# Optimization experiments

Measured on AMD Instinct MI355X. Metric: run time of the kernel, lower is better.

Reference implementation:

```python
import jax, jax.numpy as jnp
import numpy as np

B, T_X, T_V, F, H, PRED_LEN = 1024, 32, 64, 128, 1024, 64


def setup_inputs() -> dict:
    key = jax.random.key(0)
    ks = jax.random.split(key, 9)
    s = 1.0 / np.sqrt(H)  # PyTorch LSTM/Linear default init range
    return {
        "x": jax.random.normal(ks[0], (B, T_X, F), jnp.float32),
        "y": jax.random.normal(ks[1], (B, PRED_LEN, F), jnp.float32),
        "v": jax.random.normal(ks[2], (B, T_V, F), jnp.float32),
        "W_ih": jax.random.uniform(ks[3], (4 * H, F), jnp.float32, -s, s),
        "W_hh": jax.random.uniform(ks[4], (4 * H, H), jnp.float32, -s, s),
        "b_ih": jax.random.uniform(ks[5], (4 * H,), jnp.float32, -s, s),
        "b_hh": jax.random.uniform(ks[6], (4 * H,), jnp.float32, -s, s),
        "W_reg": jax.random.uniform(ks[7], (F, H), jnp.float32, -s, s),
        "b_reg": jax.random.uniform(ks[8], (F,), jnp.float32, -s, s),
    }


def _lstm_cell(v, h, c, W_ih, W_hh, b):
    # PyTorch gate order: i, f, g, o
    gates = v @ W_ih.T + h @ W_hh.T + b  # [B, 4H]
    i, f, g, o = jnp.split(gates, 4, axis=-1)
    c = jax.nn.sigmoid(f) * c + jax.nn.sigmoid(i) * jnp.tanh(g)
    h = jax.nn.sigmoid(o) * jnp.tanh(c)
    return h, c


def reference(x, y, v, W_ih, W_hh, b_ih, b_hh, W_reg, b_reg):
    # config.scale_x_m / scale_v_m treated as identity (external, undefined).
    b = b_ih + b_hh
    x_last = x[:, -1, :]  # last observed step, [B, F]

    # --- encoder: run LSTM over the full v sequence ---
    v_seq = jnp.transpose(v, (1, 0, 2))  # [T_V, B, F]
    h0 = jnp.zeros((x.shape[0], H), x.dtype)

    def enc_step(carry, vt):
        h, c = carry
        h, c = _lstm_cell(vt, h, c, W_ih, W_hh, b)
        return (h, c), None

    (h, c), _ = jax.lax.scan(enc_step, (h0, h0), v_seq)

    # reg applied to all LSTM outputs then last step taken == reg(h_T)
    v1 = h @ W_reg.T + b_reg  # [B, F]
    x1 = x_last + v1

    def dec_step(carry, _):
        vcur, h, c, xcur = carry
        h, c = _lstm_cell(vcur, h, c, W_ih, W_hh, b)
        vnew = h @ W_reg.T + b_reg
        xnew = xcur + vnew  # x accumulates increments (x += in torch)
        return (vnew, h, c, xnew), xnew

    _, xs = jax.lax.scan(dec_step, (v1, h, c, x1), None, length=PRED_LEN - 1)

    output = jnp.concatenate([x1[None], xs], axis=0)  # [PRED_LEN, B, F]
    y_out = jnp.transpose(y, (1, 0, 2))  # scale_x_m(y.permute(1,0,2)) = identity
    return output, y_out
```

## Files before the change

kernel.cpp:

```cpp
#include <hip/hip_runtime.h>
#include <cstdint>
#include <cstddef>


typedef unsigned short u16;
typedef __bf16 bf16x8 __attribute__((ext_vector_type(8)));
typedef float f32x4 __attribute__((ext_vector_type(4)));

#define DI __device__ __forceinline__

DI u16 f2bf(float x) {
    uint32_t u = __float_as_uint(x);
    u += 0x7fffu + ((u >> 16) & 1u);
    return (u16)(u >> 16);
}
DI float sigm(float x) { return 1.0f / (1.0f + __expf(-x)); }
DI float tanh_(float x) {
    float e = __expf(-2.0f * fabsf(x));
    float r = (1.0f - e) / (1.0f + e);
    return copysignf(r, x);
}

DI void gld16(const void* g, void* l) {
    __builtin_amdgcn_global_load_lds(
        (__attribute__((address_space(1))) void*)(uintptr_t)(g),
        (__attribute__((address_space(3))) void*)(l), 16, 0, 0);
}

DI f32x4 mfma16(bf16x8 a, bf16x8 b, f32x4 c) {
    return __builtin_amdgcn_mfma_f32_16x16x32_bf16(a, b, c, 0, 0, 0);
}

__global__ __launch_bounds__(512, 4)
void lstm_step(const u16* __restrict__ A,
               const u16* __restrict__ W,
               int ldw, int kt0, int ntk,
               const float* __restrict__ bias,
               float* __restrict__ cst,
               u16* __restrict__ Aout,
               u16* __restrict__ hall,
               const float* __restrict__ vsrc)
{
    __shared__ __align__(16) u16 As[2][4096];
    __shared__ __align__(16) u16 Bs[2][8192];
    const int tid  = threadIdx.x;
    const int lane = tid & 63, wave = tid >> 6;
    const int wm = wave >> 1, wn = wave & 1;
    const int l15 = lane & 15, l4 = lane >> 4;

    const int id = blockIdx.x;
    const int xcd = id & 7, slot = id >> 3;
    const int bx = xcd * 4 + (slot >> 4);
    const int by = slot & 15;
    const int u0 = bx << 5, b0 = by << 6;

    f32x4 acc[4] = {};

    const u16* asrc = A + (size_t)(b0 + (wave & 3) * 16 + l15) * 1152
                        + (wave >> 2) * 32 + l4 * 8;
    const u16* bsrc[2];
#pragma unroll
    for (int i = 0; i < 2; ++i) {
        const int fi = i * 8 + wave;
        const int ks = fi >> 3, uh = (fi >> 2) & 1, g = fi & 3;
        bsrc[i] = W + (size_t)(g * 1024 + u0 + uh * 16 + l15) * ldw
                    + ks * 32 + l4 * 8;
    }

#define STAGE(kt, buf)                                                        \
    {                                                                         \
        const size_t ko = (size_t)(kt) * 64;                                  \
        gld16(asrc + ko, (char*)&As[buf][0] + (wave << 10));                  \
        gld16(bsrc[0] + ko, (char*)&Bs[buf][0] + (wave << 10));               \
        gld16(bsrc[1] + ko, (char*)&Bs[buf][0] + ((8 + wave) << 10));         \
    }

    STAGE(kt0, 0);
    __syncthreads();
    int buf = 0;
    for (int kt = kt0; kt < ntk; ++kt) {
        if (kt + 1 < ntk) STAGE(kt + 1, buf ^ 1);
#pragma unroll
        for (int ks = 0; ks < 2; ++ks) {
            const bf16x8 af = *(const bf16x8*)((const char*)&As[buf][0] +
                              (((ks * 4 + wm) * 64 + lane) << 4));
            bf16x8 bfr[4];
#pragma unroll
            for (int g = 0; g < 4; ++g)
                bfr[g] = *(const bf16x8*)((const char*)&Bs[buf][0] +
                         (((ks * 8 + wn * 4 + g) * 64 + lane) << 4));
#pragma unroll
            for (int g = 0; g < 4; ++g)
                acc[g] = mfma16(af, bfr[g], acc[g]);
        }
        __syncthreads();
        buf ^= 1;
    }
#undef STAGE

    const int u = u0 + wn * 16 + l15;
    const float bi = bias[u],        bff = bias[1024 + u],
                bg = bias[2048 + u], bo  = bias[3072 + u];
    const int brow = b0 + wm * 16 + l4 * 4;
#pragma unroll
    for (int j = 0; j < 4; ++j) {
        const int b = brow + j;
        const size_t ci = (size_t)b * 1024 + u;
        const float cold = cst[ci];
        const float xi = acc[0][j] + bi;
        const float xf = acc[1][j] + bff;
        const float xg = acc[2][j] + bg;
        const float xo = acc[3][j] + bo;
        const float cn = sigm(xf) * cold + sigm(xi) * tanh_(xg);
        const float hn = sigm(xo) * tanh_(cn);
        cst[ci] = cn;
        const u16 hb = f2bf(hn);
        Aout[(size_t)b * 1152 + u] = hb;
        if (hall) hall[(size_t)b * 1024 + u] = hb;
    }

    if (vsrc != nullptr && bx == 0) {
        for (int s = tid; s < 2048; s += 512) {
            const int bl = s >> 5, f4 = s & 31;
            const float4 vv = *(const float4*)(vsrc + (size_t)(b0 + bl) * 8192 + f4 * 4);
            ushort4 ov = make_ushort4(f2bf(vv.x), f2bf(vv.y), f2bf(vv.z), f2bf(vv.w));
            *(ushort4*)(Aout + (size_t)(b0 + bl) * 1152 + 1024 + f4 * 4) = ov;
        }
    }
}

__global__ __launch_bounds__(256)
void gemm_nt(const u16* __restrict__ A, int lda,
             const u16* __restrict__ Bw, float* __restrict__ C)
{
    __shared__ __align__(16) u16 As[128 * 64];
    __shared__ __align__(16) u16 Bs[128 * 64];
    const int tid = threadIdx.x, lane = tid & 63, wave = tid >> 6;
    const int wm = wave >> 1, wn = wave & 1;
    const int l15 = lane & 15, l4 = lane >> 4;
    const size_t row0 = (size_t)blockIdx.x * 128;

    f32x4 acc[4][4] = {};
    const u16* asrc[4];
    const u16* bsrc[4];
#pragma unroll
    for (int i = 0; i < 4; ++i) {
        int fi = i * 4 + wave;
        int ks = fi >> 3, rib = fi & 7;
        int r = rib * 16 + l15, k = ks * 32 + l4 * 8;
        asrc[i] = A + (row0 + r) * (size_t)lda + k;
        bsrc[i] = Bw + (size_t)r * 1024 + k;
    }
    for (int kt = 0; kt < 16; ++kt) {
#pragma unroll
        for (int i = 0; i < 4; ++i) {
            gld16(asrc[i] + kt * 64, (char*)As + ((i * 256 + wave * 64) << 4));
            gld16(bsrc[i] + kt * 64, (char*)Bs + ((i * 256 + wave * 64) << 4));
        }
        __syncthreads();
#pragma unroll
        for (int ks = 0; ks < 2; ++ks) {
            bf16x8 af[4], bfr[4];
#pragma unroll
            for (int t = 0; t < 4; ++t) {
                af[t]  = *(const bf16x8*)((const char*)As + (((ks * 8 + wm * 4 + t) * 64 + lane) << 4));
                bfr[t] = *(const bf16x8*)((const char*)Bs + (((ks * 8 + wn * 4 + t) * 64 + lane) << 4));
            }
#pragma unroll
            for (int mi = 0; mi < 4; ++mi)
#pragma unroll
                for (int ni = 0; ni < 4; ++ni)
                    acc[mi][ni] = mfma16(af[mi], bfr[ni], acc[mi][ni]);
        }
        __syncthreads();
    }
#pragma unroll
    for (int mi = 0; mi < 4; ++mi)
#pragma unroll
        for (int ni = 0; ni < 4; ++ni) {
            const int r = wm * 64 + mi * 16 + l4 * 4;
            const int cc = wn * 64 + ni * 16 + l15;
#pragma unroll
            for (int j = 0; j < 4; ++j)
                C[(row0 + r + j) * 128 + cc] = acc[mi][ni][j];
        }
}


__global__ __launch_bounds__(256)
void scan_out(const float* __restrict__ Vall, const float* __restrict__ x,
              const float* __restrict__ breg, float* __restrict__ out)
{
    const int idx = blockIdx.x * 256 + threadIdx.x;
    const int b = idx >> 7, f = idx & 127;
    const float br = breg[f];
    float acc = x[(size_t)b * 4096 + 31 * 128 + f];
    for (int k = 0; k < 64; ++k) {
        acc += Vall[(size_t)k * 131072 + idx] + br;
        out[(size_t)k * 131072 + idx] = acc;
    }
}

__global__ __launch_bounds__(256)
void transpose_y(const float* __restrict__ y, float* __restrict__ out2)
{
    const int idx = blockIdx.x * 256 + threadIdx.x;
    const int f4 = idx & 31;
    const int rest = idx >> 5;
    const int b = rest & 1023, p = rest >> 10;
    const float4 vv = *(const float4*)(y + ((size_t)b * 64 + p) * 128 + f4 * 4);
    *(float4*)(out2 + ((size_t)p * 1024 + b) * 128 + f4 * 4) = vv;
}

__global__ __launch_bounds__(256)
void conv_wcat(const float* __restrict__ Whh, const float* __restrict__ Wih,
               u16* __restrict__ Wcat)
{
    const int idx = blockIdx.x * 256 + threadIdx.x;
    const int j = idx / 288, r = idx % 288;
    const float4 vv = (r < 256)
        ? *(const float4*)(Whh + (size_t)j * 1024 + r * 4)
        : *(const float4*)(Wih + (size_t)j * 128 + (r - 256) * 4);
    ushort4 ov = make_ushort4(f2bf(vv.x), f2bf(vv.y), f2bf(vv.z), f2bf(vv.w));
    *(ushort4*)(Wcat + (size_t)j * 1152 + r * 4) = ov;
}

__global__ __launch_bounds__(256)
void conv_wreg(const float* __restrict__ Wreg, u16* __restrict__ Wregb)
{
    const int idx = blockIdx.x * 256 + threadIdx.x;
    const float4 vv = *(const float4*)(Wreg + (size_t)idx * 4);
    ushort4 ov = make_ushort4(f2bf(vv.x), f2bf(vv.y), f2bf(vv.z), f2bf(vv.w));
    *(ushort4*)(Wregb + (size_t)idx * 4) = ov;
}

__global__ __launch_bounds__(256)
void prep_wdec(const float* __restrict__ Whh, const float* __restrict__ Wih,
               const float* __restrict__ Wreg, const float* __restrict__ bih,
               const float* __restrict__ bhh, const float* __restrict__ breg,
               u16* __restrict__ Wdec, float* __restrict__ bcomb,
               float* __restrict__ bdec)
{
    __shared__ float wih[16][128];
    const int jt = blockIdx.x >> 2, ut = blockIdx.x & 3;
    const int j0 = jt * 16;
    const int u = ut * 256 + threadIdx.x;
    for (int s = threadIdx.x; s < 2048; s += 256)
        wih[s >> 7][s & 127] = Wih[(size_t)(j0 + (s >> 7)) * 128 + (s & 127)];
    __syncthreads();
    float acc[16];
#pragma unroll
    for (int j = 0; j < 16; ++j) acc[j] = Whh[(size_t)(j0 + j) * 1024 + u];
    for (int f = 0; f < 128; ++f) {
        const float wr = Wreg[(size_t)f * 1024 + u];
#pragma unroll
        for (int j = 0; j < 16; ++j) acc[j] += wih[j][f] * wr;
    }
#pragma unroll
    for (int j = 0; j < 16; ++j)
        Wdec[(size_t)(j0 + j) * 1024 + u] = f2bf(acc[j]);
    if (ut == 0 && threadIdx.x < 16) {
        const int j = j0 + threadIdx.x;
        float a = bih[j] + bhh[j];
        bcomb[j] = a;
        for (int f = 0; f < 128; ++f) a += wih[threadIdx.x][f] * breg[f];
        bdec[j] = a;
    }
}

__global__ __launch_bounds__(256)
void init_acat(const float* __restrict__ v, u16* __restrict__ Acat)
{
    const int idx = blockIdx.x * 256 + threadIdx.x;
    const int b = idx >> 5, f4 = idx & 31;
    const float4 vv = *(const float4*)(v + (size_t)b * 8192 + f4 * 4);
    ushort4 ov = make_ushort4(f2bf(vv.x), f2bf(vv.y), f2bf(vv.z), f2bf(vv.w));
    *(ushort4*)(Acat + (size_t)b * 1152 + 1024 + f4 * 4) = ov;
}


extern "C" void kernel_launch(void* const* d_in, const int* in_sizes, int n_in,
                              void* d_out, int out_size, void* d_ws, size_t ws_size,
                              hipStream_t stream)
{
    const float* x    = (const float*)d_in[0];
    const float* y    = (const float*)d_in[1];
    const float* v    = (const float*)d_in[2];
    const float* Wih  = (const float*)d_in[3];
    const float* Whh  = (const float*)d_in[4];
    const float* bih  = (const float*)d_in[5];
    const float* bhh  = (const float*)d_in[6];
    const float* Wreg = (const float*)d_in[7];
    const float* breg = (const float*)d_in[8];
    float* out = (float*)d_out;
    char* ws = (char*)d_ws;

    u16*   Wcat  = (u16*)(ws + 0);
    u16*   Wdec  = (u16*)(ws + 9437184);
    u16*   Wregb = (u16*)(ws + 17825792);
    float* bcomb = (float*)(ws + 18087936);
    float* bdec  = (float*)(ws + 18104320);
    u16*   Ac0   = (u16*)(ws + 18120704);
    u16*   Ac1   = (u16*)(ws + 20480000);
    float* cst   = (float*)(ws + 22839296);
    u16*   Hall  = (u16*)(ws + 27033600);
    float* Vall  = out;
    u16* Ac[2] = {Ac0, Ac1};

    const bool batched = ws_size >= (size_t)27033600 + 134217728;

    hipMemsetAsync(cst, 0, 4194304, stream);
    hipMemsetAsync(Ac0, 0, 2359296, stream);
    prep_wdec<<<1024, 256, 0, stream>>>(Whh, Wih, Wreg, bih, bhh, breg,
                                        Wdec, bcomb, bdec);
    conv_wcat<<<4608, 256, 0, stream>>>(Whh, Wih, Wcat);
    conv_wreg<<<128, 256, 0, stream>>>(Wreg, Wregb);
    init_acat<<<128, 256, 0, stream>>>(v, Ac0);
    transpose_y<<<8192, 256, 0, stream>>>(y, out + 8388608);

    for (int t = 0; t < 64; ++t) {
        lstm_step<<<512, 512, 0, stream>>>(
            Ac[t & 1], Wcat, 1152, (t == 0) ? 16 : 0, 18, bcomb, cst,
            Ac[(t + 1) & 1],
            (batched && t == 63) ? Hall : (u16*)nullptr,
            (t < 63) ? (v + (size_t)(t + 1) * 128) : (const float*)nullptr);
    }
    if (!batched)
        gemm_nt<<<8, 256, 0, stream>>>(Ac[0], 1152, Wregb, Vall);

    for (int k = 1; k < 64; ++k) {
        lstm_step<<<512, 512, 0, stream>>>(
            Ac[(k + 1) & 1], Wdec, 1024, 0, 16, bdec, cst, Ac[k & 1],
            batched ? (Hall + (size_t)k * 1048576) : (u16*)nullptr,
            (const float*)nullptr);
        if (!batched)
            gemm_nt<<<8, 256, 0, stream>>>(Ac[k & 1], 1152, Wregb,
                                           Vall + (size_t)k * 131072);
    }
    if (batched)
        gemm_nt<<<512, 256, 0, stream>>>(Hall, 1024, Wregb, Vall);

    scan_out<<<512, 256, 0, stream>>>(Vall, x, breg, out);
}
```

Baseline: 3.916 ms.

## Enlarge LSTM step tile to 128x128 with triple-buffered LDS pipeline

The per-step LSTM GEMM now uses 256-thread blocks that each compute a 128-batch by 32-unit (times 4 gates) tile, giving each wave a 4x4 grid of MFMA accumulators instead of 1x4. Global-to-LDS loads are triple-buffered, with explicit vmcnt waits and one barrier per k-tile, replacing double buffering with two barriers. The aim is more MFMA work per loaded fragment and better overlap of loads with compute. In exchange the grid is halved to 256 blocks, LDS use rises to 96KB per block, and register pressure grows, so fewer waves are resident on each CU.

```diff
diff --git a/kernel.cpp b/kernel.cpp
--- a/kernel.cpp
+++ b/kernel.cpp
@@ -31,7 +31,7 @@
     return __builtin_amdgcn_mfma_f32_16x16x32_bf16(a, b, c, 0, 0, 0);
 }
 
-__global__ __launch_bounds__(512, 4)
+__global__ __launch_bounds__(256, 1)
 void lstm_step(const u16* __restrict__ A,
                const u16* __restrict__ W,
                int ldw, int kt0, int ntk,
@@ -41,8 +41,7 @@
                u16* __restrict__ hall,
                const float* __restrict__ vsrc)
 {
-    __shared__ __align__(16) u16 As[2][4096];
-    __shared__ __align__(16) u16 Bs[2][8192];
+    __shared__ __align__(16) u16 S[3][16384];
     const int tid  = threadIdx.x;
     const int lane = tid & 63, wave = tid >> 6;
     const int wm = wave >> 1, wn = wave & 1;
@@ -50,77 +49,93 @@
 
     const int id = blockIdx.x;
     const int xcd = id & 7, slot = id >> 3;
-    const int bx = xcd * 4 + (slot >> 4);
-    const int by = slot & 15;
-    const int u0 = bx << 5, b0 = by << 6;
-
-    f32x4 acc[4] = {};
-
-    const u16* asrc = A + (size_t)(b0 + (wave & 3) * 16 + l15) * 1152
-                        + (wave >> 2) * 32 + l4 * 8;
-    const u16* bsrc[2];
-#pragma unroll
-    for (int i = 0; i < 2; ++i) {
-        const int fi = i * 8 + wave;
-        const int ks = fi >> 3, uh = (fi >> 2) & 1, g = fi & 3;
-        bsrc[i] = W + (size_t)(g * 1024 + u0 + uh * 16 + l15) * ldw
-                    + ks * 32 + l4 * 8;
-    }
-
-#define STAGE(kt, buf)                                                        \
+    const int bx = xcd * 4 + (slot >> 3);
+    const int by = slot & 7;
+    const int u0 = bx << 5, b0 = by << 7;
+
+    f32x4 acc[4][4] = {};
+
+    const u16* src[8];
+#pragma unroll
+    for (int i = 0; i < 8; ++i) {
+        const int c = wave * 8 + i;
+        const int ks = c & 1;
+        if (c < 16) {
+            const int mf = c >> 1;
+            src[i] = A + (size_t)(b0 + mf * 16 + l15) * 1152 + ks * 32 + l4 * 8;
+        } else {
+            const int nf = (c - 16) >> 1, g = nf >> 1, us = nf & 1;
+            src[i] = W + (size_t)(g * 1024 + u0 + us * 16 + l15) * ldw
+                       + ks * 32 + l4 * 8;
+        }
+    }
+
+#define STAGE(kt, bufi)                                                       \
     {                                                                         \
         const size_t ko = (size_t)(kt) * 64;                                  \
-        gld16(asrc + ko, (char*)&As[buf][0] + (wave << 10));                  \
-        gld16(bsrc[0] + ko, (char*)&Bs[buf][0] + (wave << 10));               \
-        gld16(bsrc[1] + ko, (char*)&Bs[buf][0] + ((8 + wave) << 10));         \
-    }
-
+        _Pragma("unroll")                                                     \
+        for (int i = 0; i < 8; ++i)                                           \
+            gld16(src[i] + ko, (char*)&S[bufi][0] + ((wave * 8 + i) << 10));  \
+    }
+
+    const int nt = ntk - kt0;
     STAGE(kt0, 0);
-    __syncthreads();
-    int buf = 0;
-    for (int kt = kt0; kt < ntk; ++kt) {
-        if (kt + 1 < ntk) STAGE(kt + 1, buf ^ 1);
+    if (nt > 1) STAGE(kt0 + 1, 1);
+
+    for (int t = 0; t < nt; ++t) {
+        if (t + 1 < nt) asm volatile("s_waitcnt vmcnt(8)" ::: "memory");
+        else            asm volatile("s_waitcnt vmcnt(0)" ::: "memory");
+        __builtin_amdgcn_sched_barrier(0);
+        __builtin_amdgcn_s_barrier();
+        __builtin_amdgcn_sched_barrier(0);
+        if (t + 2 < nt) STAGE(kt0 + t + 2, (t + 2) % 3);
+
+        const char* Sb = (const char*)&S[t % 3][0];
 #pragma unroll
         for (int ks = 0; ks < 2; ++ks) {
-            const bf16x8 af = *(const bf16x8*)((const char*)&As[buf][0] +
-                              (((ks * 4 + wm) * 64 + lane) << 4));
-            bf16x8 bfr[4];
+            bf16x8 af[4], bfr[4];
+#pragma unroll
+            for (int mi = 0; mi < 4; ++mi)
+                af[mi] = *(const bf16x8*)(Sb +
+                         ((((wm * 4 + mi) * 2 + ks) << 10) + (lane << 4)));
 #pragma unroll
             for (int g = 0; g < 4; ++g)
-                bfr[g] = *(const bf16x8*)((const char*)&Bs[buf][0] +
-                         (((ks * 8 + wn * 4 + g) * 64 + lane) << 4));
+                bfr[g] = *(const bf16x8*)(Sb +
+                         (((16 + (g * 2 + wn) * 2 + ks) << 10) + (lane << 4)));
 #pragma unroll
             for (int g = 0; g < 4; ++g)
-                acc[g] = mfma16(af, bfr[g], acc[g]);
-        }
-        __syncthreads();
-        buf ^= 1;
+#pragma unroll
+                for (int mi = 0; mi < 4; ++mi)
+                    acc[g][mi] = mfma16(af[mi], bfr[g], acc[g][mi]);
+        }
     }
 #undef STAGE
 
     const int u = u0 + wn * 16 + l15;
     const float bi = bias[u],        bff = bias[1024 + u],
                 bg = bias[2048 + u], bo  = bias[3072 + u];
-    const int brow = b0 + wm * 16 + l4 * 4;
-#pragma unroll
-    for (int j = 0; j < 4; ++j) {
-        const int b = brow + j;
-        const size_t ci = (size_t)b * 1024 + u;
-        const float cold = cst[ci];
-        const float xi = acc[0][j] + bi;
-        const float xf = acc[1][j] + bff;
-        const float xg = acc[2][j] + bg;
-        const float xo = acc[3][j] + bo;
-        const float cn = sigm(xf) * cold + sigm(xi) * tanh_(xg);
-        const float hn = sigm(xo) * tanh_(cn);
-        cst[ci] = cn;
-        const u16 hb = f2bf(hn);
-        Aout[(size_t)b * 1152 + u] = hb;
-        if (hall) hall[(size_t)b * 1024 + u] = hb;
+#pragma unroll
+    for (int mi = 0; mi < 4; ++mi) {
+#pragma unroll
+        for (int j = 0; j < 4; ++j) {
+            const int b = b0 + wm * 64 + mi * 16 + l4 * 4 + j;
+            const size_t ci = (size_t)b * 1024 + u;
+            const float cold = cst[ci];
+            const float xi = acc[0][mi][j] + bi;
+            const float xf = acc[1][mi][j] + bff;
+            const float xg = acc[2][mi][j] + bg;
+            const float xo = acc[3][mi][j] + bo;
+            const float cn = sigm(xf) * cold + sigm(xi) * tanh_(xg);
+            const float hn = sigm(xo) * tanh_(cn);
+            cst[ci] = cn;
+            const u16 hb = f2bf(hn);
+            Aout[(size_t)b * 1152 + u] = hb;
+            if (hall) hall[(size_t)b * 1024 + u] = hb;
+        }
     }
 
     if (vsrc != nullptr && bx == 0) {
-        for (int s = tid; s < 2048; s += 512) {
+        for (int s = tid; s < 4096; s += 256) {
             const int bl = s >> 5, f4 = s & 31;
             const float4 vv = *(const float4*)(vsrc + (size_t)(b0 + bl) * 8192 + f4 * 4);
             ushort4 ov = make_ushort4(f2bf(vv.x), f2bf(vv.y), f2bf(vv.z), f2bf(vv.w));
@@ -319,7 +334,7 @@
     transpose_y<<<8192, 256, 0, stream>>>(y, out + 8388608);
 
     for (int t = 0; t < 64; ++t) {
-        lstm_step<<<512, 512, 0, stream>>>(
+        lstm_step<<<256, 256, 0, stream>>>(
             Ac[t & 1], Wcat, 1152, (t == 0) ? 16 : 0, 18, bcomb, cst,
             Ac[(t + 1) & 1],
             (batched && t == 63) ? Hall : (u16*)nullptr,
@@ -329,7 +344,7 @@
         gemm_nt<<<8, 256, 0, stream>>>(Ac[0], 1152, Wregb, Vall);
 
     for (int k = 1; k < 64; ++k) {
-        lstm_step<<<512, 512, 0, stream>>>(
+        lstm_step<<<256, 256, 0, stream>>>(
             Ac[(k + 1) & 1], Wdec, 1024, 0, 16, bdec, cst, Ac[k & 1],
             batched ? (Hall + (size_t)k * 1048576) : (u16*)nullptr,
             (const float*)nullptr);
```

Measured after the change: 3.548 ms. 9.4% less time.
